# Performance work log

Hardware: AMD Instinct MI355X
Metric: run time of the kernel (lower is better)

The kernel has to match this reference:

```python
import jax, jax.numpy as jnp
import numpy as np

RADIUS = 3
OUT = 16
EPS = 1e-5


def setup_inputs() -> dict:
    key = jax.random.key(0)
    ks = jax.random.split(key, 20)
    N, E, EL, IN, OUT2 = 100000, 1600000, 6400000, 16, 2 * OUT
    inp = {
        "x": jax.random.normal(ks[0], (N, IN), jnp.float32),
        "y": jax.random.normal(ks[1], (E, IN), jnp.float32),
        "deg_g": jax.random.uniform(ks[2], (N, 1), jnp.float32),
        "deg_lg": jax.random.uniform(ks[3], (E, 1), jnp.float32),
        "theta_W": jax.random.normal(ks[4], (3 + RADIUS, OUT2, IN), jnp.float32) * 0.1,
        "theta_b": jax.random.normal(ks[5], (3 + RADIUS, OUT2), jnp.float32) * 0.1,
        "gamma_W": jax.random.normal(ks[6], (3 + RADIUS, OUT2, IN), jnp.float32) * 0.1,
        "gamma_b": jax.random.normal(ks[7], (3 + RADIUS, OUT2), jnp.float32) * 0.1,
        "bn_x_w": jnp.ones((OUT,), jnp.float32),
        "bn_x_b": jnp.zeros((OUT,), jnp.float32),
        "bn_y_w": jnp.ones((OUT,), jnp.float32),
        "bn_y_b": jnp.zeros((OUT,), jnp.float32),
        "src_g": jax.random.randint(ks[8], (E,), 0, N, jnp.int32),
        "dst_g": jax.random.randint(ks[9], (E,), 0, N, jnp.int32),
        "src_lg": jax.random.randint(ks[10], (EL,), 0, E, jnp.int32),
        "dst_lg": jax.random.randint(ks[11], (EL,), 0, E, jnp.int32),
        "eid2nid": jax.random.randint(ks[12], (E,), 0, N, jnp.int32),
    }
    return inp


def _spmm(z, src, dst, n):
    # copy_src + sum: out[v] = sum_{(u,v) in edges} z[u]
    return jax.ops.segment_sum(z[src], dst, num_segments=n)


def _aggregate(z, src, dst, n, radius):
    zl = []
    z = _spmm(z, src, dst, n)
    zl.append(z)
    for i in range(radius - 1):
        for _ in range(2 ** i):
            z = _spmm(z, src, dst, n)
        zl.append(z)
    return zl


def _lin(z, W, b):
    return z @ W.T + b


def _bn(h, w, b):
    m = h.mean(axis=0)
    v = h.var(axis=0)  # biased, as torch BN training normalization
    return (h - m) * jax.lax.rsqrt(v + EPS) * w + b


def reference(x, y, deg_g, deg_lg, theta_W, theta_b, gamma_W, gamma_b,
              bn_x_w, bn_x_b, bn_y_w, bn_y_b,
              src_g, dst_g, src_lg, dst_lg, eid2nid):
    N, E = x.shape[0], y.shape[0]
    # edge -> source-node feature gather (F.embedding)
    xy = x[eid2nid]
    # node branch
    x_list = [_lin(z, theta_W[3 + i], theta_b[3 + i])
              for i, z in enumerate(_aggregate(x, src_g, dst_g, N, RADIUS))]
    yx = jax.ops.segment_sum(y, dst_g, num_segments=N)  # copy_edge + sum
    xn = (_lin(x, theta_W[0], theta_b[0])
          + _lin(deg_g * x, theta_W[1], theta_b[1])
          + sum(x_list)
          + _lin(yx, theta_W[2], theta_b[2]))
    x_out = _bn(xn[:, :OUT] + jax.nn.relu(xn[:, OUT:]), bn_x_w, bn_x_b)
    # line-graph (edge) branch
    y_list = [_lin(z, gamma_W[3 + i], gamma_b[3 + i])
              for i, z in enumerate(_aggregate(y, src_lg, dst_lg, E, RADIUS))]
    xy_agg = _spmm(xy, src_lg, dst_lg, E)
    yn = (_lin(y, gamma_W[0], gamma_b[0])
          + _lin(deg_lg * y, gamma_W[1], gamma_b[1])
          + sum(y_list)
          + _lin(xy_agg, gamma_W[2], gamma_b[2]))
    y_out = _bn(yn[:, :OUT] + jax.nn.relu(yn[:, OUT:]), bn_y_w, bn_y_b)
    return (x_out, y_out)
```

## Files before the change

kernel.cpp:

```cpp
#include <hip/hip_runtime.h>
#include <stdint.h>

__device__ __forceinline__ float bf2f(unsigned short u){
  union { unsigned int i; float f; } x; x.i = ((unsigned int)u) << 16; return x.f;
}
__device__ __forceinline__ unsigned short f2bf(float f){
  union { float f; unsigned int i; } x; x.f = f;
  unsigned int r = x.i + 0x7fff + ((x.i >> 16) & 1);
  return (unsigned short)(r >> 16);
}
__device__ __forceinline__ void unpack8(uint4 v, float* o){
  o[0]=bf2f((unsigned short)(v.x)); o[1]=bf2f((unsigned short)(v.x>>16));
  o[2]=bf2f((unsigned short)(v.y)); o[3]=bf2f((unsigned short)(v.y>>16));
  o[4]=bf2f((unsigned short)(v.z)); o[5]=bf2f((unsigned short)(v.z>>16));
  o[6]=bf2f((unsigned short)(v.w)); o[7]=bf2f((unsigned short)(v.w>>16));
}
__device__ __forceinline__ uint4 pack8(const float* f){
  uint4 v;
  v.x = (unsigned)f2bf(f[0]) | ((unsigned)f2bf(f[1])<<16);
  v.y = (unsigned)f2bf(f[2]) | ((unsigned)f2bf(f[3])<<16);
  v.z = (unsigned)f2bf(f[4]) | ((unsigned)f2bf(f[5])<<16);
  v.w = (unsigned)f2bf(f[6]) | ((unsigned)f2bf(f[7])<<16);
  return v;
}
__device__ __forceinline__ void loadrow16_bf(const unsigned short* p, float* in){
  uint4 a = *(const uint4*)p; uint4 b = *(const uint4*)(p+8);
  unpack8(a, in); unpack8(b, in+8);
}
__device__ __forceinline__ void loadrow16_f32(const float* p, float* in){
  float4 a = *(const float4*)p;      float4 b = *(const float4*)(p+4);
  float4 c = *(const float4*)(p+8);  float4 d = *(const float4*)(p+12);
  in[0]=a.x; in[1]=a.y; in[2]=a.z; in[3]=a.w;
  in[4]=b.x; in[5]=b.y; in[6]=b.z; in[7]=b.w;
  in[8]=c.x; in[9]=c.y; in[10]=c.z; in[11]=c.w;
  in[12]=d.x; in[13]=d.y; in[14]=d.z; in[15]=d.w;
}

__global__ void k_f2b(const float* __restrict__ src, unsigned short* __restrict__ dst, long n8){
  long t = (long)blockIdx.x*blockDim.x + threadIdx.x;
  if (t >= n8) return;
  const float* p = src + t*8;
  float4 a = *(const float4*)p; float4 b = *(const float4*)(p+4);
  float f[8] = {a.x,a.y,a.z,a.w,b.x,b.y,b.z,b.w};
  *(uint4*)(dst + t*8) = pack8(f);
}


__global__ void __launch_bounds__(256) k_bcount(
    const int* __restrict__ dst, int n, int chunk, int shift, int nb,
    int* __restrict__ bkt_cnt){
  extern __shared__ int hist[];
  for (int b = threadIdx.x; b < nb; b += 256) hist[b] = 0;
  __syncthreads();
  int i0 = blockIdx.x * chunk;
  int iend = min(i0 + chunk, n);
  for (int i = i0 + threadIdx.x; i < iend; i += 256)
    atomicAdd(&hist[dst[i] >> shift], 1);
  __syncthreads();
  for (int b = threadIdx.x; b < nb; b += 256){
    int h = hist[b];
    if (h) atomicAdd(&bkt_cnt[b], h);
  }
}

__global__ void k_bscan(const int* __restrict__ bkt_cnt, int* __restrict__ bkt_base,
                        int* __restrict__ bcur, int nb){
  __shared__ int s[256];
  __shared__ int carry;
  if (threadIdx.x==0) carry = 0;
  __syncthreads();
  for (int base=0; base<nb; base+=256){
    int i = base + threadIdx.x;
    int v = (i<nb) ? bkt_cnt[i] : 0;
    s[threadIdx.x] = v; __syncthreads();
    for (int off=1; off<256; off<<=1){
      int t = (threadIdx.x>=off) ? s[threadIdx.x-off] : 0;
      __syncthreads();
      s[threadIdx.x] += t;
      __syncthreads();
    }
    int excl = s[threadIdx.x] - v + carry;
    if (i<nb){ bkt_base[i] = excl; bcur[i*16] = excl; }
    int tot = s[255];
    __syncthreads();
    if (threadIdx.x==0) carry += tot;
    __syncthreads();
  }
  if (threadIdx.x==0) bkt_base[nb] = carry;
}

template<int PAY>
__global__ void __launch_bounds__(256) k_scatter(
    const int* __restrict__ src, const int* __restrict__ dst, int n, int chunk,
    int shift, int nb, int* __restrict__ bcur, int* __restrict__ out){
  extern __shared__ int sh[];
  int* hist = sh;
  int* base = sh + nb;
  for (int b = threadIdx.x; b < nb; b += 256) hist[b] = 0;
  __syncthreads();
  int i0 = blockIdx.x * chunk;
  int iend = min(i0 + chunk, n);
  for (int i = i0 + threadIdx.x; i < iend; i += 256)
    atomicAdd(&hist[dst[i] >> shift], 1);
  __syncthreads();
  for (int b = threadIdx.x; b < nb; b += 256){
    int h = hist[b];
    base[b] = h ? atomicAdd(&bcur[b*16], h) : 0;
  }
  __syncthreads();
  for (int i = i0 + threadIdx.x; i < iend; i += 256){
    int d = dst[i];
    int b = d >> shift;
    int p = atomicAdd(&base[b], 1);
    if (PAY == 2) *(int2*)(out + (size_t)p*2) = make_int2(d, src[i]);
    else          *(int4*)(out + (size_t)p*4) = make_int4(d, src[i], i, 0);
  }
}

template<bool EID, int RLOG>
__global__ void __launch_bounds__(256) k_place2(
    const int* __restrict__ bkt_base, const int* __restrict__ binned,
    int nrows, int* __restrict__ rowptr,
    int* __restrict__ colA, int* __restrict__ colB){
  constexpr int R = 1 << RLOG;
  constexpr int K = R / 256;
  __shared__ int cnt[R];
  __shared__ int s[256];
  int rowBase = blockIdx.x << RLOG;
  int nr = min(R, nrows - rowBase);
  int beg = bkt_base[blockIdx.x], end = bkt_base[blockIdx.x+1];
  #pragma unroll
  for (int k=0;k<K;k++) cnt[threadIdx.x + k*256] = 0;
  __syncthreads();
  for (int i = beg + threadIdx.x; i < end; i += 256){
    int d = EID ? ((const int4*)binned)[i].x : ((const int2*)binned)[i].x;
    atomicAdd(&cnt[d & (R-1)], 1);
  }
  __syncthreads();
  int myBase = threadIdx.x * K;
  int part = 0;
  #pragma unroll
  for (int k=0;k<K;k++) part += cnt[myBase+k];
  s[threadIdx.x] = part; __syncthreads();
  for (int off=1; off<256; off<<=1){
    int t = (threadIdx.x>=off) ? s[threadIdx.x-off] : 0;
    __syncthreads();
    s[threadIdx.x] += t;
    __syncthreads();
  }
  int run = s[threadIdx.x] - part + beg;
  #pragma unroll
  for (int k=0;k<K;k++){
    int idx = myBase + k;
    int c = cnt[idx];
    cnt[idx] = run;
    if (idx < nr) rowptr[rowBase + idx] = run;
    run += c;
  }
  if (blockIdx.x == gridDim.x-1 && threadIdx.x == 255) rowptr[nrows] = end;
  __syncthreads();
  for (int i = beg + threadIdx.x; i < end; i += 256){
    if (EID){
      int4 v = ((const int4*)binned)[i];
      int p = atomicAdd(&cnt[v.x & (R-1)], 1);
      colA[p] = v.y; colB[p] = v.z;
    } else {
      int2 v = ((const int2*)binned)[i];
      int p = atomicAdd(&cnt[v.x & (R-1)], 1);
      colA[p] = v.y;
    }
  }
}

__global__ void __launch_bounds__(256) k_spmm(
    const int* __restrict__ rowptr, const int* __restrict__ col,
    const int* __restrict__ remap,
    const unsigned short* __restrict__ src, unsigned short* __restrict__ out, int nrows){
  int t = blockIdx.x*256 + threadIdx.x;
  int row = t >> 1, half = t & 1;
  if (row >= nrows) return;
  int beg = rowptr[row], end = rowptr[row+1];
  float acc[8] = {0,0,0,0,0,0,0,0};
  const unsigned short* sp = src + (half<<3);
  for (int i=beg; i<end; ++i){
    int c = col[i];
    if (remap) c = remap[c];
    uint4 v = *(const uint4*)(sp + ((size_t)c<<4));
    float f[8]; unpack8(v, f);
    #pragma unroll
    for (int j=0;j<8;j++) acc[j] += f[j];
  }
  *(uint4*)(out + ((size_t)row<<4) + (half<<3)) = pack8(acc);
}

__device__ __forceinline__ void accum16(float* acc, const float* in, const float* __restrict__ w){
  #pragma unroll
  for (int o=0;o<32;o++){
    float a = acc[o];
    #pragma unroll
    for (int i=0;i<16;i++) a = fmaf(in[i], w[o*16+i], a);
    acc[o] = a;
  }
}

__global__ void __launch_bounds__(256) k_final(
    const float* __restrict__ base, const float* __restrict__ deg,
    const unsigned short* __restrict__ agg2, const unsigned short* __restrict__ z1,
    const unsigned short* __restrict__ z2, const unsigned short* __restrict__ z4,
    const float* __restrict__ W, const float* __restrict__ Bb,
    float* __restrict__ hout, int nrows){
  int r = blockIdx.x*256 + threadIdx.x;
  if (r >= nrows) return;
  float acc[32];
  #pragma unroll
  for (int o=0;o<32;o++){
    float b = 0.f;
    #pragma unroll
    for (int k=0;k<6;k++) b += Bb[k*32 + o];
    acc[o] = b;
  }
  float in[16];
  loadrow16_f32(base + (size_t)r*16, in);
  accum16(acc, in, W);
  float dg = deg[r];
  #pragma unroll
  for (int i=0;i<16;i++) in[i] *= dg;
  accum16(acc, in, W + 512);
  loadrow16_bf(agg2 + (size_t)r*16, in); accum16(acc, in, W + 1024);
  loadrow16_bf(z1   + (size_t)r*16, in); accum16(acc, in, W + 1536);
  loadrow16_bf(z2   + (size_t)r*16, in); accum16(acc, in, W + 2048);
  loadrow16_bf(z4   + (size_t)r*16, in); accum16(acc, in, W + 2560);
  float* op = hout + (size_t)r*16;
  float4 o0 = make_float4(acc[0]+fmaxf(acc[16],0.f), acc[1]+fmaxf(acc[17],0.f),
                          acc[2]+fmaxf(acc[18],0.f), acc[3]+fmaxf(acc[19],0.f));
  float4 o1 = make_float4(acc[4]+fmaxf(acc[20],0.f), acc[5]+fmaxf(acc[21],0.f),
                          acc[6]+fmaxf(acc[22],0.f), acc[7]+fmaxf(acc[23],0.f));
  float4 o2 = make_float4(acc[8]+fmaxf(acc[24],0.f), acc[9]+fmaxf(acc[25],0.f),
                          acc[10]+fmaxf(acc[26],0.f), acc[11]+fmaxf(acc[27],0.f));
  float4 o3 = make_float4(acc[12]+fmaxf(acc[28],0.f), acc[13]+fmaxf(acc[29],0.f),
                          acc[14]+fmaxf(acc[30],0.f), acc[15]+fmaxf(acc[31],0.f));
  *(float4*)(op)      = o0;
  *(float4*)(op + 4)  = o1;
  *(float4*)(op + 8)  = o2;
  *(float4*)(op + 12) = o3;
}

__global__ void __launch_bounds__(256) k_red(
    const float* __restrict__ h, int nrows, float* __restrict__ stats){
  __shared__ float redS[4][16];
  __shared__ float redQ[4][16];
  float ssum[16], ssq[16];
  #pragma unroll
  for (int c=0;c<16;c++){ ssum[c]=0.f; ssq[c]=0.f; }
  for (long r = (long)blockIdx.x*256 + threadIdx.x; r < nrows; r += (long)gridDim.x*256){
    float in[16];
    loadrow16_f32(h + r*16, in);
    #pragma unroll
    for (int c=0;c<16;c++){ ssum[c] += in[c]; ssq[c] += in[c]*in[c]; }
  }
  int lane = threadIdx.x & 63, wid = threadIdx.x >> 6;
  #pragma unroll
  for (int c=0;c<16;c++){
    float s = ssum[c], q = ssq[c];
    for (int off=32; off; off>>=1){ s += __shfl_xor(s, off, 64); q += __shfl_xor(q, off, 64); }
    if (lane==0){ redS[wid][c] = s; redQ[wid][c] = q; }
  }
  __syncthreads();
  if (threadIdx.x < 16){
    float s=0.f, q=0.f;
    #pragma unroll
    for (int w4=0; w4<4; w4++){ s += redS[w4][threadIdx.x]; q += redQ[w4][threadIdx.x]; }
    atomicAdd(&stats[threadIdx.x], s);
    atomicAdd(&stats[16 + threadIdx.x], q);
  }
}

__global__ void k_stats(const float* __restrict__ st,
                        const float* __restrict__ wx, const float* __restrict__ bx,
                        const float* __restrict__ wy, const float* __restrict__ by,
                        float* __restrict__ prm, int nx, int ny){
  int c = threadIdx.x;
  if (c < 16){
    float m  = st[c]/(float)nx;
    float v  = st[16+c]/(float)nx - m*m;
    float sc = wx[c] * rsqrtf(v + 1e-5f);
    prm[c] = sc; prm[16+c] = bx[c] - m*sc;
    float m2  = st[32+c]/(float)ny;
    float v2  = st[48+c]/(float)ny - m2*m2;
    float sc2 = wy[c] * rsqrtf(v2 + 1e-5f);
    prm[32+c] = sc2; prm[48+c] = by[c] - m2*sc2;
  }
}

__global__ void k_norm(float* __restrict__ out, const float* __restrict__ prm,
                       long nx, long ntot){
  long g = ((long)blockIdx.x*256 + threadIdx.x) * 8;
  if (g >= ntot) return;
  const float* p = (g < nx) ? prm : prm + 32;
  int cbase = (int)(g & 15);
  float4 a = *(float4*)(out + g);
  float4 b = *(float4*)(out + g + 4);
  float f[8] = {a.x,a.y,a.z,a.w,b.x,b.y,b.z,b.w};
  #pragma unroll
  for (int j=0;j<8;j++){ int c = cbase + j; f[j] = f[j]*p[c] + p[16+c]; }
  *(float4*)(out + g)     = make_float4(f[0],f[1],f[2],f[3]);
  *(float4*)(out + g + 4) = make_float4(f[4],f[5],f[6],f[7]);
}

extern "C" void kernel_launch(void* const* d_in, const int* in_sizes, int n_in,
                              void* d_out, int out_size, void* d_ws, size_t ws_size,
                              hipStream_t stream){
  const float* x      = (const float*)d_in[0];
  const float* y      = (const float*)d_in[1];
  const float* deg_g  = (const float*)d_in[2];
  const float* deg_lg = (const float*)d_in[3];
  const float* thW    = (const float*)d_in[4];
  const float* thB    = (const float*)d_in[5];
  const float* gaW    = (const float*)d_in[6];
  const float* gaB    = (const float*)d_in[7];
  const float* bnxw   = (const float*)d_in[8];
  const float* bnxb   = (const float*)d_in[9];
  const float* bnyw   = (const float*)d_in[10];
  const float* bnyb   = (const float*)d_in[11];
  const int* src_g   = (const int*)d_in[12];
  const int* dst_g   = (const int*)d_in[13];
  const int* src_lg  = (const int*)d_in[14];
  const int* dst_lg  = (const int*)d_in[15];
  const int* eid2nid = (const int*)d_in[16];

  const int N  = in_sizes[2];
  const int E  = in_sizes[3];
  const int EL = in_sizes[14];

  char* w = (char*)d_ws;
  auto alloc = [&](size_t bytes)->void*{
    void* p = (void*)w; w += (bytes + 255) & ~(size_t)255; return p;
  };
  int* g_rowptr   = (int*)alloc((size_t)(N+1)*4);
  int* g_col_src  = (int*)alloc((size_t)E*4);
  int* g_col_eid  = (int*)alloc((size_t)E*4);
  int* lg_rowptr  = (int*)alloc((size_t)(E+1)*4);
  int* lg_col     = (int*)alloc((size_t)EL*4);
  int* bcur       = (int*)alloc((size_t)1024*16*4);
  int* bkt_cnt_g  = (int*)alloc(1024*4);
  int* bkt_base_g = (int*)alloc(1025*4);
  int* bkt_cnt_l  = (int*)alloc(1024*4);
  int* bkt_base_l = (int*)alloc(1025*4);
  float* stats    = (float*)alloc(64*4);
  float* prm      = (float*)alloc(64*4);
  unsigned short* xb  = (unsigned short*)alloc((size_t)N*16*2);
  unsigned short* nz1 = (unsigned short*)alloc((size_t)N*16*2);
  unsigned short* nz2 = (unsigned short*)alloc((size_t)N*16*2);
  unsigned short* nz3 = (unsigned short*)alloc((size_t)N*16*2);
  unsigned short* nz4 = (unsigned short*)alloc((size_t)N*16*2);
  unsigned short* nyx = (unsigned short*)alloc((size_t)N*16*2);
  unsigned short* eb1 = (unsigned short*)alloc((size_t)E*16*2);
  unsigned short* eb2 = (unsigned short*)alloc((size_t)E*16*2);
  unsigned short* eb3 = (unsigned short*)alloc((size_t)E*16*2);
  unsigned short* yb  = (unsigned short*)alloc((size_t)E*16*2);
  unsigned short* eb4 = yb;
  int* binned_g = (int*)eb1;
  int* binned_l = (int*)eb2;

  hipMemsetAsync(bkt_cnt_g, 0, 1024*4, stream);
  hipMemsetAsync(bkt_cnt_l, 0, 1024*4, stream);
  hipMemsetAsync(stats, 0, 64*4, stream);

  long nx8 = (long)N*16/8, ny8 = (long)E*16/8;
  k_f2b<<<(int)((nx8+255)/256), 256, 0, stream>>>(x, xb, nx8);
  k_f2b<<<(int)((ny8+255)/256), 256, 0, stream>>>(y, yb, ny8);

  const int RLOG_G = 8;
  int nb_g = (N + (1<<RLOG_G) - 1) >> RLOG_G;
  k_bcount<<<(E+8191)/8192, 256, (size_t)nb_g*4, stream>>>(
      dst_g, E, 8192, RLOG_G, nb_g, bkt_cnt_g);
  k_bscan<<<1, 256, 0, stream>>>(bkt_cnt_g, bkt_base_g, bcur, nb_g);
  k_scatter<4><<<(E+8191)/8192, 256, (size_t)2*nb_g*4, stream>>>(
      src_g, dst_g, E, 8192, RLOG_G, nb_g, bcur, binned_g);
  k_place2<true, RLOG_G><<<nb_g, 256, 0, stream>>>(
      bkt_base_g, binned_g, N, g_rowptr, g_col_src, g_col_eid);

  const int RLOG_L = 11;
  int nb_l = (E + (1<<RLOG_L) - 1) >> RLOG_L;
  k_bcount<<<(EL+16383)/16384, 256, (size_t)nb_l*4, stream>>>(
      dst_lg, EL, 16384, RLOG_L, nb_l, bkt_cnt_l);
  k_bscan<<<1, 256, 0, stream>>>(bkt_cnt_l, bkt_base_l, bcur, nb_l);
  k_scatter<2><<<(EL+16383)/16384, 256, (size_t)2*nb_l*4, stream>>>(
      src_lg, dst_lg, EL, 16384, RLOG_L, nb_l, bcur, binned_l);
  k_place2<false, RLOG_L><<<nb_l, 256, 0, stream>>>(
      bkt_base_l, binned_l, E, lg_rowptr, lg_col, (int*)nullptr);

  int gs = (2*N+255)/256;
  int es = (2*E+255)/256;
  k_spmm<<<es, 256, 0, stream>>>(lg_rowptr, lg_col, nullptr, yb,  eb1, E);
  k_spmm<<<gs, 256, 0, stream>>>(g_rowptr, g_col_eid, nullptr, yb, nyx, N);
  k_spmm<<<gs, 256, 0, stream>>>(g_rowptr, g_col_src, nullptr, xb,  nz1, N);
  k_spmm<<<gs, 256, 0, stream>>>(g_rowptr, g_col_src, nullptr, nz1, nz2, N);
  k_spmm<<<gs, 256, 0, stream>>>(g_rowptr, g_col_src, nullptr, nz2, nz3, N);
  k_spmm<<<gs, 256, 0, stream>>>(g_rowptr, g_col_src, nullptr, nz3, nz4, N);
  k_spmm<<<es, 256, 0, stream>>>(lg_rowptr, lg_col, nullptr, eb1, eb2, E);
  k_spmm<<<es, 256, 0, stream>>>(lg_rowptr, lg_col, nullptr, eb2, eb3, E);
  k_spmm<<<es, 256, 0, stream>>>(lg_rowptr, lg_col, nullptr, eb3, eb4, E);
  k_spmm<<<es, 256, 0, stream>>>(lg_rowptr, lg_col, eid2nid, xb,  eb3, E);

  float* outp = (float*)d_out;
  k_final<<<(N+255)/256, 256, 0, stream>>>(x, deg_g, nyx, nz1, nz2, nz4,
                                           thW, thB, outp, N);
  k_final<<<(E+255)/256, 256, 0, stream>>>(y, deg_lg, eb3, eb1, eb2, eb4,
                                           gaW, gaB, outp + (size_t)N*16, E);

  k_red<<<512, 256, 0, stream>>>(outp, N, stats);
  k_red<<<512, 256, 0, stream>>>(outp + (size_t)N*16, E, stats + 32);
  k_stats<<<1, 64, 0, stream>>>(stats, bnxw, bnxb, bnyw, bnyb, prm, N, E);
  long ntot = (long)(N + E) * 16;
  k_norm<<<(int)((ntot/8 + 255)/256), 256, 0, stream>>>(outp, prm, (long)N*16, ntot);
}
```

Before: 1.654 ms.

## Move final linear layers onto bf16 MFMA with split weights and unroll SpMM by two

The per-row scalar FMA final projection becomes a wave-level MFMA kernel. It processes 16-row tiles with K=96 split into three bf16 MFMA steps, and the weights are split into hi/lo bf16 halves to keep accuracy close to fp32. The base and degree-scaled inputs are now rounded to bf16 before the multiply, which adds some precision loss. Separately, the SpMM gather loop is unrolled by two with dual accumulators, and the remap branch becomes a template parameter, so more gathers are in flight at once.

```diff
diff --git a/kernel.cpp b/kernel.cpp
--- a/kernel.cpp
+++ b/kernel.cpp
@@ -1,5 +1,8 @@
 #include <hip/hip_runtime.h>
 #include <stdint.h>
+
+typedef __attribute__((ext_vector_type(8))) short bfx8;
+typedef __attribute__((ext_vector_type(4))) float f32x4;
 
 __device__ __forceinline__ float bf2f(unsigned short u){
   union { unsigned int i; float f; } x; x.i = ((unsigned int)u) << 16; return x.f;
@@ -23,10 +26,6 @@
   v.w = (unsigned)f2bf(f[6]) | ((unsigned)f2bf(f[7])<<16);
   return v;
 }
-__device__ __forceinline__ void loadrow16_bf(const unsigned short* p, float* in){
-  uint4 a = *(const uint4*)p; uint4 b = *(const uint4*)(p+8);
-  unpack8(a, in); unpack8(b, in+8);
-}
 __device__ __forceinline__ void loadrow16_f32(const float* p, float* in){
   float4 a = *(const float4*)p;      float4 b = *(const float4*)(p+4);
   float4 c = *(const float4*)(p+8);  float4 d = *(const float4*)(p+12);
@@ -35,6 +34,13 @@
   in[8]=c.x; in[9]=c.y; in[10]=c.z; in[11]=c.w;
   in[12]=d.x; in[13]=d.y; in[14]=d.z; in[15]=d.w;
 }
+__device__ __forceinline__ bfx8 f32x8_to_bf(const float* p, float m){
+  float4 a = *(const float4*)p; float4 b = *(const float4*)(p+4);
+  bfx8 r;
+  r[0]=(short)f2bf(a.x*m); r[1]=(short)f2bf(a.y*m); r[2]=(short)f2bf(a.z*m); r[3]=(short)f2bf(a.w*m);
+  r[4]=(short)f2bf(b.x*m); r[5]=(short)f2bf(b.y*m); r[6]=(short)f2bf(b.z*m); r[7]=(short)f2bf(b.w*m);
+  return r;
+}
 
 __global__ void k_f2b(const float* __restrict__ src, unsigned short* __restrict__ dst, long n8){
   long t = (long)blockIdx.x*blockDim.x + threadIdx.x;
@@ -44,7 +50,6 @@
   float f[8] = {a.x,a.y,a.z,a.w,b.x,b.y,b.z,b.w};
   *(uint4*)(dst + t*8) = pack8(f);
 }
-
 
 __global__ void __launch_bounds__(256) k_bcount(
     const int* __restrict__ dst, int n, int chunk, int shift, int nb,
@@ -172,6 +177,7 @@
   }
 }
 
+template<bool REMAP>
 __global__ void __launch_bounds__(256) k_spmm(
     const int* __restrict__ rowptr, const int* __restrict__ col,
     const int* __restrict__ remap,
@@ -181,68 +187,99 @@
   if (row >= nrows) return;
   int beg = rowptr[row], end = rowptr[row+1];
   float acc[8] = {0,0,0,0,0,0,0,0};
+  float acc2[8] = {0,0,0,0,0,0,0,0};
   const unsigned short* sp = src + (half<<3);
-  for (int i=beg; i<end; ++i){
+  int i = beg;
+  for (; i+2 <= end; i += 2){
+    int c0 = col[i], c1 = col[i+1];
+    if (REMAP){ c0 = remap[c0]; c1 = remap[c1]; }
+    uint4 v0 = *(const uint4*)(sp + ((size_t)c0<<4));
+    uint4 v1 = *(const uint4*)(sp + ((size_t)c1<<4));
+    float f0[8], f1[8]; unpack8(v0, f0); unpack8(v1, f1);
+    #pragma unroll
+    for (int j=0;j<8;j++){ acc[j] += f0[j]; acc2[j] += f1[j]; }
+  }
+  if (i < end){
     int c = col[i];
-    if (remap) c = remap[c];
+    if (REMAP) c = remap[c];
     uint4 v = *(const uint4*)(sp + ((size_t)c<<4));
     float f[8]; unpack8(v, f);
     #pragma unroll
     for (int j=0;j<8;j++) acc[j] += f[j];
   }
+  #pragma unroll
+  for (int j=0;j<8;j++) acc[j] += acc2[j];
   *(uint4*)(out + ((size_t)row<<4) + (half<<3)) = pack8(acc);
 }
 
-__device__ __forceinline__ void accum16(float* acc, const float* in, const float* __restrict__ w){
-  #pragma unroll
-  for (int o=0;o<32;o++){
-    float a = acc[o];
-    #pragma unroll
-    for (int i=0;i<16;i++) a = fmaf(in[i], w[o*16+i], a);
-    acc[o] = a;
-  }
-}
-
-__global__ void __launch_bounds__(256) k_final(
+__global__ void __launch_bounds__(256) k_final_mfma(
     const float* __restrict__ base, const float* __restrict__ deg,
-    const unsigned short* __restrict__ agg2, const unsigned short* __restrict__ z1,
-    const unsigned short* __restrict__ z2, const unsigned short* __restrict__ z4,
+    const unsigned short* __restrict__ s2, const unsigned short* __restrict__ s3,
+    const unsigned short* __restrict__ s4, const unsigned short* __restrict__ s5,
     const float* __restrict__ W, const float* __restrict__ Bb,
     float* __restrict__ hout, int nrows){
-  int r = blockIdx.x*256 + threadIdx.x;
-  if (r >= nrows) return;
-  float acc[32];
-  #pragma unroll
-  for (int o=0;o<32;o++){
-    float b = 0.f;
-    #pragma unroll
-    for (int k=0;k<6;k++) b += Bb[k*32 + o];
-    acc[o] = b;
-  }
-  float in[16];
-  loadrow16_f32(base + (size_t)r*16, in);
-  accum16(acc, in, W);
-  float dg = deg[r];
-  #pragma unroll
-  for (int i=0;i<16;i++) in[i] *= dg;
-  accum16(acc, in, W + 512);
-  loadrow16_bf(agg2 + (size_t)r*16, in); accum16(acc, in, W + 1024);
-  loadrow16_bf(z1   + (size_t)r*16, in); accum16(acc, in, W + 1536);
-  loadrow16_bf(z2   + (size_t)r*16, in); accum16(acc, in, W + 2048);
-  loadrow16_bf(z4   + (size_t)r*16, in); accum16(acc, in, W + 2560);
-  float* op = hout + (size_t)r*16;
-  float4 o0 = make_float4(acc[0]+fmaxf(acc[16],0.f), acc[1]+fmaxf(acc[17],0.f),
-                          acc[2]+fmaxf(acc[18],0.f), acc[3]+fmaxf(acc[19],0.f));
-  float4 o1 = make_float4(acc[4]+fmaxf(acc[20],0.f), acc[5]+fmaxf(acc[21],0.f),
-                          acc[6]+fmaxf(acc[22],0.f), acc[7]+fmaxf(acc[23],0.f));
-  float4 o2 = make_float4(acc[8]+fmaxf(acc[24],0.f), acc[9]+fmaxf(acc[25],0.f),
-                          acc[10]+fmaxf(acc[26],0.f), acc[11]+fmaxf(acc[27],0.f));
-  float4 o3 = make_float4(acc[12]+fmaxf(acc[28],0.f), acc[13]+fmaxf(acc[29],0.f),
-                          acc[14]+fmaxf(acc[30],0.f), acc[15]+fmaxf(acc[31],0.f));
-  *(float4*)(op)      = o0;
-  *(float4*)(op + 4)  = o1;
-  *(float4*)(op + 8)  = o2;
-  *(float4*)(op + 12) = o3;
+  int lane = threadIdx.x & 63;
+  int l15 = lane & 15;
+  int quad = lane >> 4;
+  int kbase = quad * 8;
+  int slocal = kbase >> 4;
+  int k0 = kbase & 15;
+
+  bfx8 bh[3][2], bl[3][2];
+  #pragma unroll
+  for (int kb=0; kb<3; ++kb){
+    int s = kb*2 + slocal;
+    #pragma unroll
+    for (int t=0;t<2;++t){
+      int o = t*16 + l15;
+      const float* wp = W + s*512 + o*16 + k0;
+      bfx8 hi, lo;
+      #pragma unroll
+      for (int j=0;j<8;j++){
+        float w0 = wp[j];
+        unsigned short h = f2bf(w0);
+        unsigned short l2 = f2bf(w0 - bf2f(h));
+        hi[j] = (short)h; lo[j] = (short)l2;
+      }
+      bh[kb][t] = hi; bl[kb][t] = lo;
+    }
+  }
+  float bias0 = 0.f, bias1 = 0.f;
+  #pragma unroll
+  for (int s=0;s<6;s++){ bias0 += Bb[s*32 + l15]; bias1 += Bb[s*32 + 16 + l15]; }
+
+  int ntiles = (nrows + 15) >> 4;
+  int wstart = (blockIdx.x<<2) + (threadIdx.x>>6);
+  int wstep  = gridDim.x<<2;
+  for (int tile = wstart; tile < ntiles; tile += wstep){
+    int R0 = tile << 4;
+    int row = R0 + l15;
+    int rowc = min(row, nrows-1);
+    size_t ro = (size_t)rowc*16 + k0;
+    float m = slocal ? deg[rowc] : 1.f;
+    bfx8 a0 = f32x8_to_bf(base + ro, m);
+    bfx8 a1 = *(const bfx8*)((slocal ? s3 : s2) + ro);
+    bfx8 a2 = *(const bfx8*)((slocal ? s5 : s4) + ro);
+    f32x4 c0 = {bias0,bias0,bias0,bias0};
+    f32x4 c1 = {bias1,bias1,bias1,bias1};
+    c0 = __builtin_amdgcn_mfma_f32_16x16x32_bf16(a0, bh[0][0], c0, 0,0,0);
+    c1 = __builtin_amdgcn_mfma_f32_16x16x32_bf16(a0, bh[0][1], c1, 0,0,0);
+    c0 = __builtin_amdgcn_mfma_f32_16x16x32_bf16(a1, bh[1][0], c0, 0,0,0);
+    c1 = __builtin_amdgcn_mfma_f32_16x16x32_bf16(a1, bh[1][1], c1, 0,0,0);
+    c0 = __builtin_amdgcn_mfma_f32_16x16x32_bf16(a2, bh[2][0], c0, 0,0,0);
+    c1 = __builtin_amdgcn_mfma_f32_16x16x32_bf16(a2, bh[2][1], c1, 0,0,0);
+    c0 = __builtin_amdgcn_mfma_f32_16x16x32_bf16(a0, bl[0][0], c0, 0,0,0);
+    c1 = __builtin_amdgcn_mfma_f32_16x16x32_bf16(a0, bl[0][1], c1, 0,0,0);
+    c0 = __builtin_amdgcn_mfma_f32_16x16x32_bf16(a1, bl[1][0], c0, 0,0,0);
+    c1 = __builtin_amdgcn_mfma_f32_16x16x32_bf16(a1, bl[1][1], c1, 0,0,0);
+    c0 = __builtin_amdgcn_mfma_f32_16x16x32_bf16(a2, bl[2][0], c0, 0,0,0);
+    c1 = __builtin_amdgcn_mfma_f32_16x16x32_bf16(a2, bl[2][1], c1, 0,0,0);
+    #pragma unroll
+    for (int j=0;j<4;j++){
+      int r = R0 + quad*4 + j;
+      if (r < nrows) hout[(size_t)r*16 + l15] = c0[j] + fmaxf(c1[j], 0.f);
+    }
+  }
 }
 
 __global__ void __launch_bounds__(256) k_red(
@@ -392,22 +429,26 @@
 
   int gs = (2*N+255)/256;
   int es = (2*E+255)/256;
-  k_spmm<<<es, 256, 0, stream>>>(lg_rowptr, lg_col, nullptr, yb,  eb1, E);
-  k_spmm<<<gs, 256, 0, stream>>>(g_rowptr, g_col_eid, nullptr, yb, nyx, N);
-  k_spmm<<<gs, 256, 0, stream>>>(g_rowptr, g_col_src, nullptr, xb,  nz1, N);
-  k_spmm<<<gs, 256, 0, stream>>>(g_rowptr, g_col_src, nullptr, nz1, nz2, N);
-  k_spmm<<<gs, 256, 0, stream>>>(g_rowptr, g_col_src, nullptr, nz2, nz3, N);
-  k_spmm<<<gs, 256, 0, stream>>>(g_rowptr, g_col_src, nullptr, nz3, nz4, N);
-  k_spmm<<<es, 256, 0, stream>>>(lg_rowptr, lg_col, nullptr, eb1, eb2, E);
-  k_spmm<<<es, 256, 0, stream>>>(lg_rowptr, lg_col, nullptr, eb2, eb3, E);
-  k_spmm<<<es, 256, 0, stream>>>(lg_rowptr, lg_col, nullptr, eb3, eb4, E);
-  k_spmm<<<es, 256, 0, stream>>>(lg_rowptr, lg_col, eid2nid, xb,  eb3, E);
+  k_spmm<false><<<es, 256, 0, stream>>>(lg_rowptr, lg_col, nullptr, yb,  eb1, E);
+  k_spmm<false><<<gs, 256, 0, stream>>>(g_rowptr, g_col_eid, nullptr, yb, nyx, N);
+  k_spmm<false><<<gs, 256, 0, stream>>>(g_rowptr, g_col_src, nullptr, xb,  nz1, N);
+  k_spmm<false><<<gs, 256, 0, stream>>>(g_rowptr, g_col_src, nullptr, nz1, nz2, N);
+  k_spmm<false><<<gs, 256, 0, stream>>>(g_rowptr, g_col_src, nullptr, nz2, nz3, N);
+  k_spmm<false><<<gs, 256, 0, stream>>>(g_rowptr, g_col_src, nullptr, nz3, nz4, N);
+  k_spmm<false><<<es, 256, 0, stream>>>(lg_rowptr, lg_col, nullptr, eb1, eb2, E);
+  k_spmm<false><<<es, 256, 0, stream>>>(lg_rowptr, lg_col, nullptr, eb2, eb3, E);
+  k_spmm<false><<<es, 256, 0, stream>>>(lg_rowptr, lg_col, nullptr, eb3, eb4, E);
+  k_spmm<true><<<es, 256, 0, stream>>>(lg_rowptr, lg_col, eid2nid, xb,  eb3, E);
 
   float* outp = (float*)d_out;
-  k_final<<<(N+255)/256, 256, 0, stream>>>(x, deg_g, nyx, nz1, nz2, nz4,
-                                           thW, thB, outp, N);
-  k_final<<<(E+255)/256, 256, 0, stream>>>(y, deg_lg, eb3, eb1, eb2, eb4,
-                                           gaW, gaB, outp + (size_t)N*16, E);
+  int ntg = ((N + 15) >> 4, 0);
+  (void)ntg;
+  int tg = (N + 15) >> 4;  int bg2 = (tg + 3) / 4;  if (bg2 > 2048) bg2 = 2048;
+  int te = (E + 15) >> 4;  int be2 = (te + 3) / 4;  if (be2 > 2048) be2 = 2048;
+  k_final_mfma<<<bg2, 256, 0, stream>>>(x, deg_g, nyx, nz1, nz2, nz4,
+                                        thW, thB, outp, N);
+  k_final_mfma<<<be2, 256, 0, stream>>>(y, deg_lg, eb3, eb1, eb2, eb4,
+                                        gaW, gaB, outp + (size_t)N*16, E);
 
   k_red<<<512, 256, 0, stream>>>(outp, N, stats);
   k_red<<<512, 256, 0, stream>>>(outp + (size_t)N*16, E, stats + 32);
```

Result: faster. 1.548 ms (-6.4%).
